# Optimization experiments

Measured on AMD Instinct MI355X. Metric: run time of the kernel, lower is better.

Reference implementation:

```python
import jax, jax.numpy as jnp
import numpy as np

INPUT_DIM = 1024
OUTPUT_DIM = 1024
SPLINE_POINTS = 4

def setup_inputs() -> dict:
    key = jax.random.key(0)
    k1, k2 = jax.random.split(key)
    x = jax.random.normal(k1, (4096, INPUT_DIM), dtype=jnp.float32)
    spline_coeffs = jax.random.normal(k2, (OUTPUT_DIM, INPUT_DIM, SPLINE_POINTS, 4), dtype=jnp.float32)
    return {"x": x, "spline_coeffs": spline_coeffs}

def reference(x, spline_coeffs):
    # Per-feature min-max normalization over the batch dim (as in the torch code,
    # where x[:, j].min()/max() are taken over the batch).
    xmin = jnp.min(x, axis=0, keepdims=True)   # [1, D]
    xmax = jnp.max(x, axis=0, keepdims=True)
    xn = (x - xmin) / (xmax - xmin)            # [B, D]

    # The original sums the cubic polynomial over all spline_points, so the
    # effective coefficients are the sum over the spline_points axis.
    c = jnp.sum(spline_coeffs, axis=2)         # [O, D, 4]

    x2 = xn * xn
    x3 = x2 * xn
    # out[b, o] = sum_d c0*x^3 + c1*x^2 + c2*x + c3
    out = (jnp.einsum('bd,od->bo', x3, c[..., 0])
           + jnp.einsum('bd,od->bo', x2, c[..., 1])
           + jnp.einsum('bd,od->bo', xn, c[..., 2])
           + jnp.sum(c[..., 3], axis=1)[None, :])
    return out
```

## Files before the change

### kernel.cpp

```cpp
#include <hip/hip_runtime.h>
#include <hip/hip_bf16.h>
#include <stdint.h>
#include <stddef.h>

typedef __bf16 bf16;
typedef __attribute__((ext_vector_type(4))) __bf16 bf16x4;
typedef __attribute__((ext_vector_type(8))) __bf16 bf16x8;
typedef __attribute__((ext_vector_type(4))) float f32x4;

#define BATCH 4096
#define DIM 1024
#define ODIM 1024
#define K3 3072

#define WS_P      0
#define WS_CB     25165824
#define WS_BIAS   31457280
#define WS_PMIN   31461376
#define WS_PMAX   31723520
#define WS_MINV   31985664
#define WS_SCALE  31989760

#define ASYNC16(g, l)                                                          \
  __builtin_amdgcn_global_load_lds(                                            \
      (__attribute__((address_space(1))) void*)(g),                            \
      (__attribute__((address_space(3))) void*)(l), 16, 0, 0)

__global__ void k_minmax_part(const float* __restrict__ x,
                              float* __restrict__ pmin,
                              float* __restrict__ pmax) {
  int col = blockIdx.x * 256 + threadIdx.x;
  int ch = blockIdx.y;
  const float* p = x + (size_t)ch * 64 * DIM + col;
  float mn = 1e30f, mx = -1e30f;
#pragma unroll 8
  for (int r = 0; r < 64; ++r) {
    float v = p[(size_t)r * DIM];
    mn = fminf(mn, v);
    mx = fmaxf(mx, v);
  }
  pmin[ch * DIM + col] = mn;
  pmax[ch * DIM + col] = mx;
}

__global__ void k_minmax_final(const float* __restrict__ pmin,
                               const float* __restrict__ pmax,
                               float* __restrict__ minv,
                               float* __restrict__ scale) {
  int col = blockIdx.x * 256 + threadIdx.x;
  float mn = 1e30f, mx = -1e30f;
#pragma unroll 8
  for (int ch = 0; ch < 64; ++ch) {
    mn = fminf(mn, pmin[ch * DIM + col]);
    mx = fmaxf(mx, pmax[ch * DIM + col]);
  }
  minv[col] = mn;
  scale[col] = 1.0f / (mx - mn);
}

__global__ void k_prep(const float* __restrict__ x,
                       const float* __restrict__ minv,
                       const float* __restrict__ scale,
                       bf16* __restrict__ P,
                       const float* __restrict__ sp,
                       bf16* __restrict__ CB,
                       float* __restrict__ bias) {
  __shared__ float red[4];
  const int t = threadIdx.x;
  if (blockIdx.x < BATCH) {
    const int b = blockIdx.x;
    const int d = t << 2;
    f32x4 xv = *(const f32x4*)(x + (size_t)b * DIM + d);
    f32x4 mn = *(const f32x4*)(minv + d);
    f32x4 sc = *(const f32x4*)(scale + d);
    bf16x4 o3, o2, o1;
#pragma unroll
    for (int j = 0; j < 4; ++j) {
      float xn = (xv[j] - mn[j]) * sc[j];
      float x2 = xn * xn;
      float x3 = x2 * xn;
      o3[j] = (bf16)x3;
      o2[j] = (bf16)x2;
      o1[j] = (bf16)xn;
    }
    size_t base = (size_t)b * K3 + d;
    *(bf16x4*)(P + base) = o3;
    *(bf16x4*)(P + base + 1024) = o2;
    *(bf16x4*)(P + base + 2048) = o1;
  } else {
    const int o = blockIdx.x - BATCH;
    const int d = t << 2;
    f32x4 s[4];
#pragma unroll
    for (int dd = 0; dd < 4; ++dd) {
      const float* p = sp + ((size_t)o * DIM + d + dd) * 16;
      f32x4 acc = *(const f32x4*)(p);
      acc += *(const f32x4*)(p + 4);
      acc += *(const f32x4*)(p + 8);
      acc += *(const f32x4*)(p + 12);
      s[dd] = acc;
    }
    size_t cb = (size_t)o * K3 + d;
    bf16x4 c0 = {(bf16)s[0][0], (bf16)s[1][0], (bf16)s[2][0], (bf16)s[3][0]};
    bf16x4 c1 = {(bf16)s[0][1], (bf16)s[1][1], (bf16)s[2][1], (bf16)s[3][1]};
    bf16x4 c2 = {(bf16)s[0][2], (bf16)s[1][2], (bf16)s[2][2], (bf16)s[3][2]};
    *(bf16x4*)(CB + cb) = c0;
    *(bf16x4*)(CB + cb + 1024) = c1;
    *(bf16x4*)(CB + cb + 2048) = c2;
    float v = s[0][3] + s[1][3] + s[2][3] + s[3][3];
#pragma unroll
    for (int off = 32; off > 0; off >>= 1) v += __shfl_down(v, off, 64);
    int lane = t & 63, w = t >> 6;
    if (lane == 0) red[w] = v;
    __syncthreads();
    if (t == 0) bias[o] = red[0] + red[1] + red[2] + red[3];
  }
}

#define BM 64
#define BN 128
#define BKE 64
__global__ __launch_bounds__(256, 2) void k_gemm(const bf16* __restrict__ P,
                                                 const bf16* __restrict__ CBm,
                                                 const float* __restrict__ bias,
                                                 float* __restrict__ out) {
  __shared__ bf16 sA[BM * BKE];
  __shared__ bf16 sB[BN * BKE];

  const int tid = threadIdx.x;
  const int wave = tid >> 6;
  const int lane = tid & 63;
  const int bm = blockIdx.x * BM;
  const int bn = blockIdx.y * BN;
  const int wr = (wave >> 1) * 32;
  const int wc = (wave & 1) * 64;

  const char* gA = (const char*)P;
  const char* gB = (const char*)CBm;
  char* lA = (char*)sA;
  char* lB = (char*)sB;
  const size_t rowbytes = (size_t)K3 * 2;

  int srowA[2], sgbA[2];
#pragma unroll
  for (int i = 0; i < 2; ++i) {
    int off = i * 4096 + tid * 16;
    int row = off >> 7;
    int q = (off >> 4) & 7;
    srowA[i] = row;
    sgbA[i] = (q ^ (row & 7)) * 16;
  }
  int srowB[4], sgbB[4];
#pragma unroll
  for (int i = 0; i < 4; ++i) {
    int off = i * 4096 + tid * 16;
    int row = off >> 7;
    int q = (off >> 4) & 7;
    srowB[i] = row;
    sgbB[i] = (q ^ (row & 7)) * 16;
  }

  f32x4 acc[2][4] = {};

  const int mrow = lane & 15;
  const int kq = lane >> 4;

  for (int k0 = 0; k0 < K3; k0 += BKE) {
    const size_t kb = (size_t)k0 * 2;
#pragma unroll
    for (int i = 0; i < 2; ++i)
      ASYNC16(gA + (size_t)(bm + srowA[i]) * rowbytes + kb + sgbA[i],
              lA + i * 4096 + wave * 1024);
#pragma unroll
    for (int i = 0; i < 4; ++i)
      ASYNC16(gB + (size_t)(bn + srowB[i]) * rowbytes + kb + sgbB[i],
              lB + i * 4096 + wave * 1024);
    __syncthreads();

    bf16x8 af[2][2], bg[2][4];
#pragma unroll
    for (int ks = 0; ks < 2; ++ks) {
#pragma unroll
      for (int i = 0; i < 2; ++i) {
        int row = wr + i * 16 + mrow;
        int sq = (ks * 4 + kq) ^ (row & 7);
        af[ks][i] = *(const bf16x8*)&sA[row * BKE + sq * 8];
      }
#pragma unroll
      for (int j = 0; j < 4; ++j) {
        int row = wc + j * 16 + mrow;
        int sq = (ks * 4 + kq) ^ (row & 7);
        bg[ks][j] = *(const bf16x8*)&sB[row * BKE + sq * 8];
      }
    }

#pragma unroll
    for (int ks = 0; ks < 2; ++ks)
#pragma unroll
      for (int i = 0; i < 2; ++i)
#pragma unroll
        for (int j = 0; j < 4; ++j)
          acc[i][j] = __builtin_amdgcn_mfma_f32_16x16x32_bf16(af[ks][i], bg[ks][j],
                                                              acc[i][j], 0, 0, 0);
    __syncthreads();
  }

  const int ccol = lane & 15;
  const int crow = (lane >> 4) * 4;
#pragma unroll
  for (int j = 0; j < 4; ++j) {
    const int col = bn + wc + j * 16 + ccol;
    const float bv = bias[col];
#pragma unroll
    for (int i = 0; i < 2; ++i) {
      const int row0 = bm + wr + i * 16 + crow;
#pragma unroll
      for (int r = 0; r < 4; ++r)
        out[(size_t)(row0 + r) * ODIM + col] = acc[i][j][r] + bv;
    }
  }
}

extern "C" void kernel_launch(void* const* d_in, const int* in_sizes, int n_in,
                              void* d_out, int out_size, void* d_ws, size_t ws_size,
                              hipStream_t stream) {
  (void)in_sizes; (void)n_in; (void)out_size; (void)ws_size;
  const float* x = (const float*)d_in[0];
  const float* sp = (const float*)d_in[1];
  float* out = (float*)d_out;
  char* ws = (char*)d_ws;

  bf16* Pm = (bf16*)(ws + WS_P);
  bf16* CBm = (bf16*)(ws + WS_CB);
  float* bias = (float*)(ws + WS_BIAS);
  float* pmin = (float*)(ws + WS_PMIN);
  float* pmax = (float*)(ws + WS_PMAX);
  float* minv = (float*)(ws + WS_MINV);
  float* scale = (float*)(ws + WS_SCALE);

  k_minmax_part<<<dim3(4, 64), 256, 0, stream>>>(x, pmin, pmax);
  k_minmax_final<<<4, 256, 0, stream>>>(pmin, pmax, minv, scale);
  k_prep<<<BATCH + ODIM, 256, 0, stream>>>(x, minv, scale, Pm, sp, CBm, bias);
  k_gemm<<<dim3(BATCH / BM, ODIM / BN), 256, 0, stream>>>(Pm, CBm, bias, out);
}
```

Before: 174.7 us.

## Double-buffer GEMM LDS tiles with async prefetch and enlarge block tile

The GEMM now uses a 128x128 block tile with two LDS buffers, so the next K-slab's global-to-LDS loads are issued before the current slab is computed. A vmcnt wait plus raw barriers replaces the pair of __syncthreads, letting load latency overlap with MFMA work. Each wave now holds a 4x4 accumulator grid, which raises register use and drops occupancy to one block per CU (launch bounds 256,1). The grid also shrinks to 256 blocks, and the min/max partial kernel switches to float4 loads over 64 blocks.

```diff
diff --git a/kernel.cpp b/kernel.cpp
--- a/kernel.cpp
+++ b/kernel.cpp
@@ -26,21 +26,33 @@
       (__attribute__((address_space(1))) void*)(g),                            \
       (__attribute__((address_space(3))) void*)(l), 16, 0, 0)
 
+#define WAIT_VM(n) __builtin_amdgcn_s_waitcnt(0x0F00 | 0x0070 | ((n)&15) | ((((n)>>4)&3)<<14))
+#define BARRIER()                     \
+  do {                                \
+    asm volatile("" ::: "memory");    \
+    __builtin_amdgcn_s_barrier();     \
+    asm volatile("" ::: "memory");    \
+  } while (0)
+
 __global__ void k_minmax_part(const float* __restrict__ x,
                               float* __restrict__ pmin,
                               float* __restrict__ pmax) {
-  int col = blockIdx.x * 256 + threadIdx.x;
-  int ch = blockIdx.y;
-  const float* p = x + (size_t)ch * 64 * DIM + col;
-  float mn = 1e30f, mx = -1e30f;
+  const int t = threadIdx.x;
+  const int ch = blockIdx.x;
+  const float* p = x + (size_t)ch * 64 * DIM + (t << 2);
+  f32x4 mn = {1e30f, 1e30f, 1e30f, 1e30f};
+  f32x4 mx = {-1e30f, -1e30f, -1e30f, -1e30f};
 #pragma unroll 8
   for (int r = 0; r < 64; ++r) {
-    float v = p[(size_t)r * DIM];
-    mn = fminf(mn, v);
-    mx = fmaxf(mx, v);
-  }
-  pmin[ch * DIM + col] = mn;
-  pmax[ch * DIM + col] = mx;
+    f32x4 v = *(const f32x4*)(p + (size_t)r * DIM);
+#pragma unroll
+    for (int j = 0; j < 4; ++j) {
+      mn[j] = fminf(mn[j], v[j]);
+      mx[j] = fmaxf(mx[j], v[j]);
+    }
+  }
+  *(f32x4*)(pmin + ch * DIM + (t << 2)) = mn;
+  *(f32x4*)(pmax + ch * DIM + (t << 2)) = mx;
 }
 
 __global__ void k_minmax_final(const float* __restrict__ pmin,
@@ -117,93 +129,92 @@
   }
 }
 
-#define BM 64
+#define BM 128
 #define BN 128
 #define BKE 64
-__global__ __launch_bounds__(256, 2) void k_gemm(const bf16* __restrict__ P,
+#define NIT (K3 / BKE)
+__global__ __launch_bounds__(256, 1) void k_gemm(const bf16* __restrict__ P,
                                                  const bf16* __restrict__ CBm,
                                                  const float* __restrict__ bias,
                                                  float* __restrict__ out) {
-  __shared__ bf16 sA[BM * BKE];
-  __shared__ bf16 sB[BN * BKE];
+  __shared__ bf16 ldsm[2][2][BM * BKE];
 
   const int tid = threadIdx.x;
   const int wave = tid >> 6;
   const int lane = tid & 63;
   const int bm = blockIdx.x * BM;
   const int bn = blockIdx.y * BN;
-  const int wr = (wave >> 1) * 32;
+  const int wr = (wave >> 1) * 64;
   const int wc = (wave & 1) * 64;
 
-  const char* gA = (const char*)P;
-  const char* gB = (const char*)CBm;
-  char* lA = (char*)sA;
-  char* lB = (char*)sB;
   const size_t rowbytes = (size_t)K3 * 2;
 
-  int srowA[2], sgbA[2];
-#pragma unroll
-  for (int i = 0; i < 2; ++i) {
-    int off = i * 4096 + tid * 16;
-    int row = off >> 7;
-    int q = (off >> 4) & 7;
-    srowA[i] = row;
-    sgbA[i] = (q ^ (row & 7)) * 16;
-  }
-  int srowB[4], sgbB[4];
+  const char* gAp[4];
+  const char* gBp[4];
+  int ldso[4];
 #pragma unroll
   for (int i = 0; i < 4; ++i) {
     int off = i * 4096 + tid * 16;
     int row = off >> 7;
     int q = (off >> 4) & 7;
-    srowB[i] = row;
-    sgbB[i] = (q ^ (row & 7)) * 16;
-  }
-
-  f32x4 acc[2][4] = {};
+    int gb = (q ^ (row & 7)) * 16;
+    gAp[i] = (const char*)P + (size_t)(bm + row) * rowbytes + gb;
+    gBp[i] = (const char*)CBm + (size_t)(bn + row) * rowbytes + gb;
+    ldso[i] = i * 4096 + wave * 1024;
+  }
+
+  f32x4 acc[4][4] = {};
 
   const int mrow = lane & 15;
   const int kq = lane >> 4;
 
-  for (int k0 = 0; k0 < K3; k0 += BKE) {
-    const size_t kb = (size_t)k0 * 2;
-#pragma unroll
-    for (int i = 0; i < 2; ++i)
-      ASYNC16(gA + (size_t)(bm + srowA[i]) * rowbytes + kb + sgbA[i],
-              lA + i * 4096 + wave * 1024);
-#pragma unroll
-    for (int i = 0; i < 4; ++i)
-      ASYNC16(gB + (size_t)(bn + srowB[i]) * rowbytes + kb + sgbB[i],
-              lB + i * 4096 + wave * 1024);
-    __syncthreads();
-
-    bf16x8 af[2][2], bg[2][4];
-#pragma unroll
-    for (int ks = 0; ks < 2; ++ks) {
-#pragma unroll
-      for (int i = 0; i < 2; ++i) {
-        int row = wr + i * 16 + mrow;
-        int sq = (ks * 4 + kq) ^ (row & 7);
-        af[ks][i] = *(const bf16x8*)&sA[row * BKE + sq * 8];
-      }
-#pragma unroll
-      for (int j = 0; j < 4; ++j) {
-        int row = wc + j * 16 + mrow;
-        int sq = (ks * 4 + kq) ^ (row & 7);
-        bg[ks][j] = *(const bf16x8*)&sB[row * BKE + sq * 8];
-      }
-    }
-
-#pragma unroll
-    for (int ks = 0; ks < 2; ++ks)
-#pragma unroll
-      for (int i = 0; i < 2; ++i)
-#pragma unroll
-        for (int j = 0; j < 4; ++j)
-          acc[i][j] = __builtin_amdgcn_mfma_f32_16x16x32_bf16(af[ks][i], bg[ks][j],
-                                                              acc[i][j], 0, 0, 0);
-    __syncthreads();
-  }
+#define STAGE(buf, kt)                                                        \
+  do {                                                                        \
+    const size_t kb_ = (size_t)(kt) * (BKE * 2);                              \
+    char* lA_ = (char*)&ldsm[buf][0][0];                                      \
+    char* lB_ = (char*)&ldsm[buf][1][0];                                      \
+    _Pragma("unroll") for (int i_ = 0; i_ < 4; ++i_)                          \
+        ASYNC16(gAp[i_] + kb_, lA_ + ldso[i_]);                               \
+    _Pragma("unroll") for (int i_ = 0; i_ < 4; ++i_)                          \
+        ASYNC16(gBp[i_] + kb_, lB_ + ldso[i_]);                               \
+  } while (0)
+
+#define COMPUTE(buf)                                                          \
+  do {                                                                        \
+    const bf16* sA_ = &ldsm[buf][0][0];                                       \
+    const bf16* sB_ = &ldsm[buf][1][0];                                       \
+    _Pragma("unroll") for (int ks = 0; ks < 2; ++ks) {                        \
+      bf16x8 af[4], bg[4];                                                    \
+      _Pragma("unroll") for (int i = 0; i < 4; ++i) {                         \
+        int row = wr + i * 16 + mrow;                                         \
+        int sq = (ks * 4 + kq) ^ (row & 7);                                   \
+        af[i] = *(const bf16x8*)&sA_[row * BKE + sq * 8];                     \
+      }                                                                       \
+      _Pragma("unroll") for (int j = 0; j < 4; ++j) {                         \
+        int row = wc + j * 16 + mrow;                                         \
+        int sq = (ks * 4 + kq) ^ (row & 7);                                   \
+        bg[j] = *(const bf16x8*)&sB_[row * BKE + sq * 8];                     \
+      }                                                                       \
+      _Pragma("unroll") for (int i = 0; i < 4; ++i)                           \
+          _Pragma("unroll") for (int j = 0; j < 4; ++j)                       \
+              acc[i][j] = __builtin_amdgcn_mfma_f32_16x16x32_bf16(            \
+                  af[i], bg[j], acc[i][j], 0, 0, 0);                          \
+    }                                                                         \
+  } while (0)
+
+  STAGE(0, 0);
+#pragma unroll 2
+  for (int kt = 0; kt < NIT - 1; ++kt) {
+    const int cur = kt & 1;
+    STAGE(cur ^ 1, kt + 1);
+    WAIT_VM(8);
+    BARRIER();
+    COMPUTE(cur);
+    BARRIER();
+  }
+  WAIT_VM(0);
+  BARRIER();
+  COMPUTE((NIT - 1) & 1);
 
   const int ccol = lane & 15;
   const int crow = (lane >> 4) * 4;
@@ -212,13 +223,15 @@
     const int col = bn + wc + j * 16 + ccol;
     const float bv = bias[col];
 #pragma unroll
-    for (int i = 0; i < 2; ++i) {
+    for (int i = 0; i < 4; ++i) {
       const int row0 = bm + wr + i * 16 + crow;
 #pragma unroll
       for (int r = 0; r < 4; ++r)
         out[(size_t)(row0 + r) * ODIM + col] = acc[i][j][r] + bv;
     }
   }
+#undef STAGE
+#undef COMPUTE
 }
 
 extern "C" void kernel_launch(void* const* d_in, const int* in_sizes, int n_in,
@@ -238,7 +251,7 @@
   float* minv = (float*)(ws + WS_MINV);
   float* scale = (float*)(ws + WS_SCALE);
 
-  k_minmax_part<<<dim3(4, 64), 256, 0, stream>>>(x, pmin, pmax);
+  k_minmax_part<<<64, 256, 0, stream>>>(x, pmin, pmax);
   k_minmax_final<<<4, 256, 0, stream>>>(pmin, pmax, minv, scale);
   k_prep<<<BATCH + ODIM, 256, 0, stream>>>(x, minv, scale, Pm, sp, CBm, bias);
   k_gemm<<<dim3(BATCH / BM, ODIM / BN), 256, 0, stream>>>(Pm, CBm, bias, out);
```

Result: faster. 163.3 us (-6.5%).
